# Kernel optimization log

Hardware: AMD Instinct MI355X
Metric: run time of the kernel (lower is better)

The kernel has to match this reference:

```python
import jax, jax.numpy as jnp
import numpy as np

N_EMB = 256
HEAD_SIZE = 256
B, T = 8, 4096

def setup_inputs() -> dict:
    key = jax.random.key(0)
    kx, kk, kq, kv = jax.random.split(key, 4)
    scale = 1.0 / np.sqrt(N_EMB)
    return {
        "x": jax.random.normal(kx, (B, T, N_EMB), dtype=jnp.float32),
        # torch Linear(n_emb, head_size, bias=False): weight [head_size, n_emb], y = x @ W.T
        # store transposed as [n_emb, head_size]
        "Wk": jax.random.normal(kk, (N_EMB, HEAD_SIZE), dtype=jnp.float32) * scale,
        "Wq": jax.random.normal(kq, (N_EMB, HEAD_SIZE), dtype=jnp.float32) * scale,
        "Wv": jax.random.normal(kv, (N_EMB, HEAD_SIZE), dtype=jnp.float32) * scale,
    }

def reference(x, Wk, Wq, Wv):
    # x: [B, T, n_emb]
    k = x @ Wk  # [B, T, H]
    q = x @ Wq
    v = x @ Wv
    T_ = x.shape[1]
    scores = jnp.einsum("bqh,bkh->bqk", q, k) * (N_EMB ** -0.5)  # note: scaled by n_emb, as in source
    causal = jnp.tril(jnp.ones((T_, T_), dtype=bool))
    scores = jnp.where(causal, scores, -jnp.inf)
    attn = jax.nn.softmax(scores, axis=-1)
    return attn @ v  # [B, T, H]
```

## Files before the change

kernel.cpp:

```cpp
#include <hip/hip_runtime.h>

#define Bn 8
#define Tn 4096
#define Dn 256
#define Mn (Bn*Tn)

typedef short bf16x8 __attribute__((ext_vector_type(8)));
typedef float f32x4 __attribute__((ext_vector_type(4)));
typedef float f32x16 __attribute__((ext_vector_type(16)));

#define P_OFF   0ul
#define ML_OFF  41943040ul
#define XB_OFF  0ul
#define WT_OFF  16777216ul
#define QKV_OFF 42598400ul

__device__ __forceinline__ unsigned short f2bf(float f) {
    union { float f; unsigned int u; } v; v.f = f;
    unsigned int r = v.u + 0x7fffu + ((v.u >> 16) & 1u);
    return (unsigned short)(r >> 16);
}
__device__ __forceinline__ float bf2f(unsigned short u) {
    union { unsigned int u; float f; } v; v.u = ((unsigned int)u) << 16;
    return v.f;
}
__device__ __forceinline__ unsigned int pk2(float a, float b) {
    return (unsigned int)f2bf(a) | ((unsigned int)f2bf(b) << 16);
}

typedef __attribute__((address_space(1))) const unsigned int* gas_p;
typedef __attribute__((address_space(3))) unsigned int* las_p;
__device__ __forceinline__ void g2lds16(const void* g, void* l) {
    __builtin_amdgcn_global_load_lds((gas_p)g, (las_p)l, 16, 0, 0);
}

__global__ void __launch_bounds__(256) cast_x_kernel(const float* __restrict__ x,
                                                     unsigned short* __restrict__ xb) {
    size_t i = (size_t)blockIdx.x * 256 + threadIdx.x;
    const float4* p = reinterpret_cast<const float4*>(x) + i * 2;
    float4 a = p[0], b = p[1];
    union { unsigned short u[8]; uint4 v; } o;
    o.u[0]=f2bf(a.x); o.u[1]=f2bf(a.y); o.u[2]=f2bf(a.z); o.u[3]=f2bf(a.w);
    o.u[4]=f2bf(b.x); o.u[5]=f2bf(b.y); o.u[6]=f2bf(b.z); o.u[7]=f2bf(b.w);
    reinterpret_cast<uint4*>(xb)[i] = o.v;
}

__global__ void __launch_bounds__(256) wt_kernel(const float* __restrict__ wq,
                                                 const float* __restrict__ wk,
                                                 const float* __restrict__ wv,
                                                 unsigned short* __restrict__ wt) {
    int idx = blockIdx.x * 256 + threadIdx.x;
    int h = idx >> 16; int r = idx & 65535;
    int k = r >> 8, n = r & 255;
    const float* src = (h == 0) ? wq : (h == 1) ? wk : wv;
    wt[h * 65536 + n * 256 + k] = f2bf(src[k * 256 + n]);
}

__global__ void __launch_bounds__(256, 2) proj_kernel(const unsigned short* __restrict__ xb,
                                                      const unsigned short* __restrict__ wt,
                                                      unsigned short* __restrict__ qkv) {
    __shared__ unsigned short wlds[256 * 40];
    int h = blockIdx.y;
    const unsigned short* wth = wt + h * 65536;
    int m0 = blockIdx.x * 64;
    int tid = threadIdx.x;
    int w = tid >> 6, lane = tid & 63;
    int c = lane & 15, g = lane >> 4;
    size_t arow = (size_t)(m0 + w * 16 + c);

    const f32x4 fz = {0.f, 0.f, 0.f, 0.f};
    f32x4 acc[16];
#pragma unroll
    for (int n = 0; n < 16; n++) acc[n] = fz;

    for (int kk = 0; kk < 8; kk++) {
        __syncthreads();
#pragma unroll
        for (int p = 0; p < 4; p++) {
            int idx = p * 256 + tid;
            int r = idx >> 2, ch = idx & 3;
            bf16x8 v = *(const bf16x8*)(wth + r * 256 + kk * 32 + ch * 8);
            *(bf16x8*)(&wlds[r * 40 + ch * 8]) = v;
        }
        __syncthreads();
        bf16x8 af = *(const bf16x8*)(xb + arow * Dn + kk * 32 + g * 8);
#pragma unroll
        for (int n = 0; n < 16; n++) {
            bf16x8 bfv = *(const bf16x8*)(&wlds[(n * 16 + c) * 40 + g * 8]);
            acc[n] = __builtin_amdgcn_mfma_f32_16x16x32_bf16(af, bfv, acc[n], 0, 0, 0);
        }
    }
    int orow0 = m0 + w * 16 + g * 4;
    if (h < 2) {
        unsigned short* out = qkv + (size_t)h * Mn * Dn;
#pragma unroll
        for (int n = 0; n < 16; n++)
#pragma unroll
            for (int r = 0; r < 4; r++)
                out[(size_t)(orow0 + r) * Dn + n * 16 + c] = f2bf(acc[n][r]);
    } else {
        unsigned short* vt = qkv + (size_t)2 * Mn * Dn;
#pragma unroll
        for (int n = 0; n < 16; n++) {
            union { unsigned short u[4]; ushort4 v4; } pk;
#pragma unroll
            for (int r = 0; r < 4; r++) pk.u[r] = f2bf(acc[n][r]);
            *(ushort4*)(vt + (size_t)(n * 16 + c) * Mn + orow0) = pk.v4;
        }
    }
}

__global__ void __launch_bounds__(256, 2) attn_kernel(const unsigned short* __restrict__ qkv,
                                                      unsigned short* __restrict__ part,
                                                      float2* __restrict__ ml) {
    __shared__ char smem[65536];

    int bid = blockIdx.x;
    int b = bid & 7;
    int r = bid >> 3;
    int qtp, cc;
    if (r < 24)      { qtp = 24 + (r & 7); cc = r >> 3; }
    else if (r < 40) { int rp = r - 24; qtp = 16 + (rp & 7); cc = rp >> 3; }
    else if (r < 48) { qtp = 8 + (r - 40); cc = 0; }
    else             { int k = r - 48; int u = k >> 2, v = k & 3; qtp = 8 * v + 7 - u; cc = v; }
    int slot = b * 80 + r;

    int tid = threadIdx.x, w = tid >> 6, lane = tid & 63;
    int lq = lane & 31, hh = lane >> 5;

    const unsigned short* Qg = qkv;
    const unsigned short* Kg = qkv + (size_t)Mn * Dn;
    const unsigned short* Vt = qkv + (size_t)2 * Mn * Dn;

    int qrow = qtp * 128 + w * 32 + lq;

    bf16x8 qf[16];
#pragma unroll
    for (int s = 0; s < 16; s++)
        qf[s] = *(const bf16x8*)(Qg + ((size_t)b * Tn + qrow) * Dn + s * 16 + hh * 8);

    f32x16 o[8];
#pragma unroll
    for (int dg = 0; dg < 8; dg++)
#pragma unroll
        for (int e = 0; e < 16; e++) o[dg][e] = 0.f;
    float m2 = -INFINITY, lsum = 0.f;

    const float C1 = 0.09016844005555897f;

    auto STAGE = [&](int bufsel, int t) {
        const unsigned short* kgb = Kg + ((size_t)b * Tn + t * 32) * Dn;
        char* kb = smem + bufsel * 32768 + w * 4096;
#pragma unroll
        for (int i = 0; i < 4; i++) {
            int row = w * 8 + i * 2 + hh;
            int chunk = lq ^ row;
            g2lds16(kgb + row * 256 + chunk * 8, kb + i * 1024);
        }
        const unsigned short* vgb = Vt + (size_t)b * Tn + t * 32;
        char* vb = smem + bufsel * 32768 + 16384 + w * 4096;
#pragma unroll
        for (int i = 0; i < 4; i++) {
            int d = w * 64 + i * 16 + (lane >> 2);
            int kvc = (lane & 3) ^ ((d >> 3) & 3);
            g2lds16(vgb + (size_t)d * Mn + kvc * 8, vb + i * 1024);
        }
    };

    auto COMPUTE = [&](int bufsel, int t) {
        int kv0 = t * 32;
        const char* klds = smem + bufsel * 32768;
        const char* vlds = klds + 16384;
        f32x16 sv;
#pragma unroll
        for (int e = 0; e < 16; e++) sv[e] = 0.f;
        __builtin_amdgcn_s_setprio(1);
#pragma unroll
        for (int s = 0; s < 16; s++) {
            bf16x8 kf = *(const bf16x8*)(klds + lq * 512 + ((2 * s + hh) ^ lq) * 16);
            sv = __builtin_amdgcn_mfma_f32_32x32x16_bf16(kf, qf[s], sv, 0, 0, 0);
        }
        __builtin_amdgcn_s_setprio(0);
        float pv[16];
        float tmax = -INFINITY;
#pragma unroll
        for (int rr = 0; rr < 16; rr++) {
            int kvl = kv0 + (rr & 3) + 8 * (rr >> 2) + 4 * hh;
            float v = sv[rr] * C1;
            v = (kvl <= qrow) ? v : -INFINITY;
            pv[rr] = v;
            tmax = fmaxf(tmax, v);
        }
        tmax = fmaxf(tmax, __shfl_xor(tmax, 32));
        float mn = m2;
        if (!__all(tmax - m2 <= 8.0f)) {
            mn = fmaxf(m2, tmax);
            float alpha = exp2f(m2 - mn);
            lsum *= alpha;
            m2 = mn;
#pragma unroll
            for (int dg = 0; dg < 8; dg++) o[dg] = o[dg] * alpha;
        }
        float ps = 0.f;
#pragma unroll
        for (int rr = 0; rr < 16; rr++) {
            pv[rr] = exp2f(pv[rr] - mn);
            ps += pv[rr];
        }
        ps += __shfl_xor(ps, 32);
        lsum += ps;
        union U4 { unsigned int u[4]; bf16x8 v; };
        U4 fr[2];
#pragma unroll
        for (int s2 = 0; s2 < 2; s2++) {
            int bidx = 8 * s2;
            unsigned int w0 = pk2(pv[bidx + 0], pv[bidx + 1]);
            unsigned int w1 = pk2(pv[bidx + 2], pv[bidx + 3]);
            unsigned int y0 = pk2(pv[bidx + 4], pv[bidx + 5]);
            unsigned int y1 = pk2(pv[bidx + 6], pv[bidx + 7]);
            unsigned int e0 = hh ? w0 : y0;
            unsigned int e1 = hh ? w1 : y1;
            unsigned int x0 = (unsigned int)__shfl_xor((int)e0, 32);
            unsigned int x1 = (unsigned int)__shfl_xor((int)e1, 32);
            fr[s2].u[0] = hh ? x0 : w0;
            fr[s2].u[1] = hh ? x1 : w1;
            fr[s2].u[2] = hh ? y0 : x0;
            fr[s2].u[3] = hh ? y1 : x1;
        }
        __builtin_amdgcn_s_setprio(1);
#pragma unroll
        for (int dg = 0; dg < 8; dg++) {
            int d = 32 * dg + lq;
            int swz = (d >> 3) & 3;
#pragma unroll
            for (int s2 = 0; s2 < 2; s2++) {
                bf16x8 vf = *(const bf16x8*)(vlds + d * 64 + ((2 * s2 + hh) ^ swz) * 16);
                o[dg] = __builtin_amdgcn_mfma_f32_32x32x16_bf16(vf, fr[s2].v, o[dg], 0, 0, 0);
            }
        }
        __builtin_amdgcn_s_setprio(0);
    };

    int t0 = cc * 32;
    int tend = min(t0 + 32, 4 * (qtp + 1));
    int cur = 0;
    STAGE(0, t0);
    __syncthreads();
    for (int t = t0; t < tend; t++) {
        if (t + 1 < tend) STAGE(cur ^ 1, t + 1);
        COMPUTE(cur, t);
        __syncthreads();
        cur ^= 1;
    }

    if (hh == 0)
        ml[(size_t)slot * 128 + w * 32 + lq] = make_float2(m2, lsum);

    uint4* pb = (uint4*)part;
#pragma unroll
    for (int dg = 0; dg < 8; dg++) {
        uint4 lo, hi2;
        lo.x = pk2(o[dg][0], o[dg][1]);  lo.y = pk2(o[dg][2], o[dg][3]);
        lo.z = pk2(o[dg][4], o[dg][5]);  lo.w = pk2(o[dg][6], o[dg][7]);
        hi2.x = pk2(o[dg][8], o[dg][9]);  hi2.y = pk2(o[dg][10], o[dg][11]);
        hi2.z = pk2(o[dg][12], o[dg][13]); hi2.w = pk2(o[dg][14], o[dg][15]);
        size_t base = (size_t)slot * 4096 + w * 1024 + dg * 128 + lane;
        pb[base] = lo;
        pb[base + 64] = hi2;
    }
}

__global__ void __launch_bounds__(256) combine_kernel(const unsigned short* __restrict__ part,
                                                      const float2* __restrict__ ml,
                                                      float* __restrict__ out) {
    __shared__ float2 mls[4][32];
    int bid = blockIdx.x;
    int b = bid & 7;
    int rest = bid >> 3;
    int qtp = rest >> 2, w = rest & 3;
    int nch = (qtp >> 3) + 1;
    int tid = threadIdx.x;

    int slots[4];
#pragma unroll
    for (int ci = 0; ci < 4; ci++) {
        int rr;
        if (ci == nch - 1)       rr = 48 + 4 * (7 - (qtp & 7)) + (qtp >> 3);
        else if (qtp >= 24)      rr = 8 * ci + (qtp - 24);
        else if (qtp >= 16)      rr = 24 + 8 * ci + (qtp - 16);
        else                     rr = 40 + (qtp - 8);
        slots[ci] = b * 80 + rr;
    }
    if (tid < nch * 32) {
        int ci = tid >> 5, qq = tid & 31;
        mls[ci][qq] = ml[(size_t)slots[ci] * 128 + w * 32 + qq];
    }
    __syncthreads();

    int dg = tid >> 5, h2 = (tid >> 4) & 1, ls = tid & 15;
    const uint4* pb = (const uint4*)part;

    for (int rd = 0; rd < 4; rd++) {
        int lane_idx = ls + 16 * rd;
        int q = lane_idx & 31, hh = lane_idx >> 5;
        float M = -INFINITY;
#pragma unroll
        for (int ci = 0; ci < 4; ci++)
            if (ci < nch) M = fmaxf(M, mls[ci][q].x);
        float L = 0.f, wgt[4];
#pragma unroll
        for (int ci = 0; ci < 4; ci++) {
            if (ci < nch) { wgt[ci] = exp2f(mls[ci][q].x - M); L += wgt[ci] * mls[ci][q].y; }
            else wgt[ci] = 0.f;
        }
        float inv = 1.f / L;
        float a[8];
#pragma unroll
        for (int e = 0; e < 8; e++) a[e] = 0.f;
#pragma unroll
        for (int ci = 0; ci < 4; ci++) {
            if (ci >= nch) break;
            uint4 u = pb[(size_t)slots[ci] * 4096 + w * 1024 + dg * 128 + h2 * 64 + lane_idx];
            float wg = wgt[ci];
            a[0] += wg * bf2f((unsigned short)(u.x & 0xffff));
            a[1] += wg * bf2f((unsigned short)(u.x >> 16));
            a[2] += wg * bf2f((unsigned short)(u.y & 0xffff));
            a[3] += wg * bf2f((unsigned short)(u.y >> 16));
            a[4] += wg * bf2f((unsigned short)(u.z & 0xffff));
            a[5] += wg * bf2f((unsigned short)(u.z >> 16));
            a[6] += wg * bf2f((unsigned short)(u.w & 0xffff));
            a[7] += wg * bf2f((unsigned short)(u.w >> 16));
        }
        size_t row = (size_t)b * Tn + qtp * 128 + w * 32 + q;
        int dbase = 32 * dg + 16 * h2 + 4 * hh;
        float4 A = {a[0] * inv, a[1] * inv, a[2] * inv, a[3] * inv};
        float4 Bv = {a[4] * inv, a[5] * inv, a[6] * inv, a[7] * inv};
        *(float4*)(out + row * 256 + dbase) = A;
        *(float4*)(out + row * 256 + dbase + 8) = Bv;
    }
}

extern "C" void kernel_launch(void* const* d_in, const int* in_sizes, int n_in,
                              void* d_out, int out_size, void* d_ws, size_t ws_size,
                              hipStream_t stream) {
    (void)in_sizes; (void)n_in; (void)out_size; (void)ws_size;
    const float* x  = (const float*)d_in[0];
    const float* wk = (const float*)d_in[1];
    const float* wq = (const float*)d_in[2];
    const float* wv = (const float*)d_in[3];
    float* outp = (float*)d_out;

    char* ws = (char*)d_ws;
    unsigned short* xb   = (unsigned short*)(ws + XB_OFF);
    unsigned short* wt   = (unsigned short*)(ws + WT_OFF);
    unsigned short* qkv  = (unsigned short*)(ws + QKV_OFF);
    unsigned short* part = (unsigned short*)(ws + P_OFF);
    float2*         mlp  = (float2*)(ws + ML_OFF);

    cast_x_kernel<<<Mn * Dn / 8 / 256, 256, 0, stream>>>(x, xb);
    wt_kernel<<<3 * 65536 / 256, 256, 0, stream>>>(wq, wk, wv, wt);
    proj_kernel<<<dim3(Mn / 64, 3), 256, 0, stream>>>(xb, wt, qkv);
    attn_kernel<<<640, 256, 0, stream>>>(qkv, part, mlp);
    combine_kernel<<<1024, 256, 0, stream>>>(part, mlp, outp);
}
```

Baseline: 201.1 us.

## Fuse x cast into projection and single-buffer V to raise attention occupancy

Removes the separate fp32-to-bf16 cast kernel for x and converts x on the fly inside the projection kernel, dropping one launch and a round trip through memory. The attention kernel keeps double-buffered K but single-buffers V, cutting shared memory from 64KB to 48KB so launch bounds allow three blocks per CU. V staging is now serialized behind the PV step with an extra barrier. The QK dot product is split into two independent accumulator chains for more MFMA overlap. The gain from extra occupancy may be offset by lost V prefetch overlap, the added sync, and register pressure at three blocks per CU.

```diff
diff --git a/kernel.cpp b/kernel.cpp
--- a/kernel.cpp
+++ b/kernel.cpp
@@ -11,7 +11,6 @@
 
 #define P_OFF   0ul
 #define ML_OFF  41943040ul
-#define XB_OFF  0ul
 #define WT_OFF  16777216ul
 #define QKV_OFF 42598400ul
 
@@ -32,17 +31,6 @@
 typedef __attribute__((address_space(3))) unsigned int* las_p;
 __device__ __forceinline__ void g2lds16(const void* g, void* l) {
     __builtin_amdgcn_global_load_lds((gas_p)g, (las_p)l, 16, 0, 0);
-}
-
-__global__ void __launch_bounds__(256) cast_x_kernel(const float* __restrict__ x,
-                                                     unsigned short* __restrict__ xb) {
-    size_t i = (size_t)blockIdx.x * 256 + threadIdx.x;
-    const float4* p = reinterpret_cast<const float4*>(x) + i * 2;
-    float4 a = p[0], b = p[1];
-    union { unsigned short u[8]; uint4 v; } o;
-    o.u[0]=f2bf(a.x); o.u[1]=f2bf(a.y); o.u[2]=f2bf(a.z); o.u[3]=f2bf(a.w);
-    o.u[4]=f2bf(b.x); o.u[5]=f2bf(b.y); o.u[6]=f2bf(b.z); o.u[7]=f2bf(b.w);
-    reinterpret_cast<uint4*>(xb)[i] = o.v;
 }
 
 __global__ void __launch_bounds__(256) wt_kernel(const float* __restrict__ wq,
@@ -56,7 +44,7 @@
     wt[h * 65536 + n * 256 + k] = f2bf(src[k * 256 + n]);
 }
 
-__global__ void __launch_bounds__(256, 2) proj_kernel(const unsigned short* __restrict__ xb,
+__global__ void __launch_bounds__(256, 2) proj_kernel(const float* __restrict__ x,
                                                       const unsigned short* __restrict__ wt,
                                                       unsigned short* __restrict__ qkv) {
     __shared__ unsigned short wlds[256 * 40];
@@ -83,11 +71,15 @@
             *(bf16x8*)(&wlds[r * 40 + ch * 8]) = v;
         }
         __syncthreads();
-        bf16x8 af = *(const bf16x8*)(xb + arow * Dn + kk * 32 + g * 8);
+        const float4* xa = (const float4*)(x + arow * Dn + kk * 32 + g * 8);
+        float4 a0 = xa[0], a1 = xa[1];
+        union { unsigned short u[8]; bf16x8 v; } af;
+        af.u[0]=f2bf(a0.x); af.u[1]=f2bf(a0.y); af.u[2]=f2bf(a0.z); af.u[3]=f2bf(a0.w);
+        af.u[4]=f2bf(a1.x); af.u[5]=f2bf(a1.y); af.u[6]=f2bf(a1.z); af.u[7]=f2bf(a1.w);
 #pragma unroll
         for (int n = 0; n < 16; n++) {
             bf16x8 bfv = *(const bf16x8*)(&wlds[(n * 16 + c) * 40 + g * 8]);
-            acc[n] = __builtin_amdgcn_mfma_f32_16x16x32_bf16(af, bfv, acc[n], 0, 0, 0);
+            acc[n] = __builtin_amdgcn_mfma_f32_16x16x32_bf16(af.v, bfv, acc[n], 0, 0, 0);
         }
     }
     int orow0 = m0 + w * 16 + g * 4;
@@ -110,10 +102,10 @@
     }
 }
 
-__global__ void __launch_bounds__(256, 2) attn_kernel(const unsigned short* __restrict__ qkv,
+__global__ void __launch_bounds__(256, 3) attn_kernel(const unsigned short* __restrict__ qkv,
                                                       unsigned short* __restrict__ part,
                                                       float2* __restrict__ ml) {
-    __shared__ char smem[65536];
+    __shared__ char smem[49152];
 
     int bid = blockIdx.x;
     int b = bid & 7;
@@ -148,17 +140,19 @@
 
     const float C1 = 0.09016844005555897f;
 
-    auto STAGE = [&](int bufsel, int t) {
+    auto STAGE_K = [&](int cb, int t) {
         const unsigned short* kgb = Kg + ((size_t)b * Tn + t * 32) * Dn;
-        char* kb = smem + bufsel * 32768 + w * 4096;
+        char* kb = smem + cb * 16384 + w * 4096;
 #pragma unroll
         for (int i = 0; i < 4; i++) {
             int row = w * 8 + i * 2 + hh;
             int chunk = lq ^ row;
             g2lds16(kgb + row * 256 + chunk * 8, kb + i * 1024);
         }
+    };
+    auto STAGE_V = [&](int t) {
         const unsigned short* vgb = Vt + (size_t)b * Tn + t * 32;
-        char* vb = smem + bufsel * 32768 + 16384 + w * 4096;
+        char* vb = smem + 32768 + w * 4096;
 #pragma unroll
         for (int i = 0; i < 4; i++) {
             int d = w * 64 + i * 16 + (lane >> 2);
@@ -167,20 +161,25 @@
         }
     };
 
-    auto COMPUTE = [&](int bufsel, int t) {
+    union U4 { unsigned int u[4]; bf16x8 v; };
+    U4 fr[2];
+
+    auto QKSM = [&](int cb, int t) {
         int kv0 = t * 32;
-        const char* klds = smem + bufsel * 32768;
-        const char* vlds = klds + 16384;
-        f32x16 sv;
-#pragma unroll
-        for (int e = 0; e < 16; e++) sv[e] = 0.f;
+        const char* klds = smem + cb * 16384;
+        f32x16 sva, svb;
+#pragma unroll
+        for (int e = 0; e < 16; e++) { sva[e] = 0.f; svb[e] = 0.f; }
         __builtin_amdgcn_s_setprio(1);
 #pragma unroll
-        for (int s = 0; s < 16; s++) {
-            bf16x8 kf = *(const bf16x8*)(klds + lq * 512 + ((2 * s + hh) ^ lq) * 16);
-            sv = __builtin_amdgcn_mfma_f32_32x32x16_bf16(kf, qf[s], sv, 0, 0, 0);
+        for (int s = 0; s < 8; s++) {
+            bf16x8 kfa = *(const bf16x8*)(klds + lq * 512 + ((2 * s + hh) ^ lq) * 16);
+            sva = __builtin_amdgcn_mfma_f32_32x32x16_bf16(kfa, qf[s], sva, 0, 0, 0);
+            bf16x8 kfb = *(const bf16x8*)(klds + lq * 512 + ((2 * (s + 8) + hh) ^ lq) * 16);
+            svb = __builtin_amdgcn_mfma_f32_32x32x16_bf16(kfb, qf[s + 8], svb, 0, 0, 0);
         }
         __builtin_amdgcn_s_setprio(0);
+        f32x16 sv = sva + svb;
         float pv[16];
         float tmax = -INFINITY;
 #pragma unroll
@@ -209,8 +208,6 @@
         }
         ps += __shfl_xor(ps, 32);
         lsum += ps;
-        union U4 { unsigned int u[4]; bf16x8 v; };
-        U4 fr[2];
 #pragma unroll
         for (int s2 = 0; s2 < 2; s2++) {
             int bidx = 8 * s2;
@@ -227,6 +224,10 @@
             fr[s2].u[2] = hh ? y0 : x0;
             fr[s2].u[3] = hh ? y1 : x1;
         }
+    };
+
+    auto PV = [&]() {
+        const char* vlds = smem + 32768;
         __builtin_amdgcn_s_setprio(1);
 #pragma unroll
         for (int dg = 0; dg < 8; dg++) {
@@ -243,14 +244,20 @@
 
     int t0 = cc * 32;
     int tend = min(t0 + 32, 4 * (qtp + 1));
-    int cur = 0;
-    STAGE(0, t0);
+    int cb = 0;
+    STAGE_K(0, t0);
+    STAGE_V(t0);
     __syncthreads();
     for (int t = t0; t < tend; t++) {
-        if (t + 1 < tend) STAGE(cur ^ 1, t + 1);
-        COMPUTE(cur, t);
+        if (t + 1 < tend) STAGE_K(cb ^ 1, t + 1);
+        QKSM(cb, t);
         __syncthreads();
-        cur ^= 1;
+        PV();
+        if (t + 1 < tend) {
+            __syncthreads();
+            STAGE_V(t + 1);
+        }
+        cb ^= 1;
     }
 
     if (hh == 0)
@@ -351,15 +358,13 @@
     float* outp = (float*)d_out;
 
     char* ws = (char*)d_ws;
-    unsigned short* xb   = (unsigned short*)(ws + XB_OFF);
     unsigned short* wt   = (unsigned short*)(ws + WT_OFF);
     unsigned short* qkv  = (unsigned short*)(ws + QKV_OFF);
     unsigned short* part = (unsigned short*)(ws + P_OFF);
     float2*         mlp  = (float2*)(ws + ML_OFF);
 
-    cast_x_kernel<<<Mn * Dn / 8 / 256, 256, 0, stream>>>(x, xb);
     wt_kernel<<<3 * 65536 / 256, 256, 0, stream>>>(wq, wk, wv, wt);
-    proj_kernel<<<dim3(Mn / 64, 3), 256, 0, stream>>>(xb, wt, qkv);
+    proj_kernel<<<dim3(Mn / 64, 3), 256, 0, stream>>>(x, wt, qkv);
     attn_kernel<<<640, 256, 0, stream>>>(qkv, part, mlp);
     combine_kernel<<<1024, 256, 0, stream>>>(part, mlp, outp);
 }
```

Result: slower. 575.9 us (+186.4%).

## Fuse x bf16 cast into projection kernel and compute Q/K/V per block

Applied to the files above, without the earlier changes.

Removes the separate cast_x kernel. Each projection block now loads its 64 fp32 rows of x, converts them to bf16 into padded LDS once, and loops over all three weight matrices instead of using a grid y-dimension of 3. This removes one launch and the bf16 round trip of x through global memory, and stops x being reread once per head. The cost is about 33KB of LDS per block for the x tile, which may limit occupancy, and one third as many blocks each doing three times the work.

```diff
diff --git a/kernel.cpp b/kernel.cpp
--- a/kernel.cpp
+++ b/kernel.cpp
@@ -11,7 +11,6 @@
 
 #define P_OFF   0ul
 #define ML_OFF  41943040ul
-#define XB_OFF  0ul
 #define WT_OFF  16777216ul
 #define QKV_OFF 42598400ul
 
@@ -32,17 +31,6 @@
 typedef __attribute__((address_space(3))) unsigned int* las_p;
 __device__ __forceinline__ void g2lds16(const void* g, void* l) {
     __builtin_amdgcn_global_load_lds((gas_p)g, (las_p)l, 16, 0, 0);
-}
-
-__global__ void __launch_bounds__(256) cast_x_kernel(const float* __restrict__ x,
-                                                     unsigned short* __restrict__ xb) {
-    size_t i = (size_t)blockIdx.x * 256 + threadIdx.x;
-    const float4* p = reinterpret_cast<const float4*>(x) + i * 2;
-    float4 a = p[0], b = p[1];
-    union { unsigned short u[8]; uint4 v; } o;
-    o.u[0]=f2bf(a.x); o.u[1]=f2bf(a.y); o.u[2]=f2bf(a.z); o.u[3]=f2bf(a.w);
-    o.u[4]=f2bf(b.x); o.u[5]=f2bf(b.y); o.u[6]=f2bf(b.z); o.u[7]=f2bf(b.w);
-    reinterpret_cast<uint4*>(xb)[i] = o.v;
 }
 
 __global__ void __launch_bounds__(256) wt_kernel(const float* __restrict__ wq,
@@ -56,56 +44,68 @@
     wt[h * 65536 + n * 256 + k] = f2bf(src[k * 256 + n]);
 }
 
-__global__ void __launch_bounds__(256, 2) proj_kernel(const unsigned short* __restrict__ xb,
+__global__ void __launch_bounds__(256, 2) proj_kernel(const float* __restrict__ x,
                                                       const unsigned short* __restrict__ wt,
                                                       unsigned short* __restrict__ qkv) {
+    __shared__ unsigned short xlds[64 * 258];
     __shared__ unsigned short wlds[256 * 40];
-    int h = blockIdx.y;
-    const unsigned short* wth = wt + h * 65536;
     int m0 = blockIdx.x * 64;
     int tid = threadIdx.x;
     int w = tid >> 6, lane = tid & 63;
     int c = lane & 15, g = lane >> 4;
-    size_t arow = (size_t)(m0 + w * 16 + c);
+
+#pragma unroll
+    for (int it = 0; it < 16; it++) {
+        int idx = it * 256 + tid;
+        int row = idx >> 6, col4 = (idx & 63) * 4;
+        float4 a = *(const float4*)(x + (size_t)(m0 + row) * Dn + col4);
+        union { unsigned short u[4]; ushort4 v4; } o4;
+        o4.u[0] = f2bf(a.x); o4.u[1] = f2bf(a.y); o4.u[2] = f2bf(a.z); o4.u[3] = f2bf(a.w);
+        *(ushort4*)(&xlds[row * 258 + col4]) = o4.v4;
+    }
+    __syncthreads();
 
     const f32x4 fz = {0.f, 0.f, 0.f, 0.f};
-    f32x4 acc[16];
-#pragma unroll
-    for (int n = 0; n < 16; n++) acc[n] = fz;
-
-    for (int kk = 0; kk < 8; kk++) {
-        __syncthreads();
-#pragma unroll
-        for (int p = 0; p < 4; p++) {
-            int idx = p * 256 + tid;
-            int r = idx >> 2, ch = idx & 3;
-            bf16x8 v = *(const bf16x8*)(wth + r * 256 + kk * 32 + ch * 8);
-            *(bf16x8*)(&wlds[r * 40 + ch * 8]) = v;
-        }
-        __syncthreads();
-        bf16x8 af = *(const bf16x8*)(xb + arow * Dn + kk * 32 + g * 8);
-#pragma unroll
-        for (int n = 0; n < 16; n++) {
-            bf16x8 bfv = *(const bf16x8*)(&wlds[(n * 16 + c) * 40 + g * 8]);
-            acc[n] = __builtin_amdgcn_mfma_f32_16x16x32_bf16(af, bfv, acc[n], 0, 0, 0);
-        }
-    }
-    int orow0 = m0 + w * 16 + g * 4;
-    if (h < 2) {
-        unsigned short* out = qkv + (size_t)h * Mn * Dn;
-#pragma unroll
-        for (int n = 0; n < 16; n++)
-#pragma unroll
-            for (int r = 0; r < 4; r++)
-                out[(size_t)(orow0 + r) * Dn + n * 16 + c] = f2bf(acc[n][r]);
-    } else {
-        unsigned short* vt = qkv + (size_t)2 * Mn * Dn;
-#pragma unroll
-        for (int n = 0; n < 16; n++) {
-            union { unsigned short u[4]; ushort4 v4; } pk;
-#pragma unroll
-            for (int r = 0; r < 4; r++) pk.u[r] = f2bf(acc[n][r]);
-            *(ushort4*)(vt + (size_t)(n * 16 + c) * Mn + orow0) = pk.v4;
+    for (int h = 0; h < 3; h++) {
+        const unsigned short* wth = wt + h * 65536;
+        f32x4 acc[16];
+#pragma unroll
+        for (int n = 0; n < 16; n++) acc[n] = fz;
+
+        for (int kk = 0; kk < 8; kk++) {
+            __syncthreads();
+#pragma unroll
+            for (int p = 0; p < 4; p++) {
+                int idx = p * 256 + tid;
+                int r = idx >> 2, ch = idx & 3;
+                bf16x8 v = *(const bf16x8*)(wth + r * 256 + kk * 32 + ch * 8);
+                *(bf16x8*)(&wlds[r * 40 + ch * 8]) = v;
+            }
+            __syncthreads();
+            bf16x8 af = *(const bf16x8*)(&xlds[(w * 16 + c) * 258 + kk * 32 + g * 8]);
+#pragma unroll
+            for (int n = 0; n < 16; n++) {
+                bf16x8 bfv = *(const bf16x8*)(&wlds[(n * 16 + c) * 40 + g * 8]);
+                acc[n] = __builtin_amdgcn_mfma_f32_16x16x32_bf16(af, bfv, acc[n], 0, 0, 0);
+            }
+        }
+        int orow0 = m0 + w * 16 + g * 4;
+        if (h < 2) {
+            unsigned short* out = qkv + (size_t)h * Mn * Dn;
+#pragma unroll
+            for (int n = 0; n < 16; n++)
+#pragma unroll
+                for (int r = 0; r < 4; r++)
+                    out[(size_t)(orow0 + r) * Dn + n * 16 + c] = f2bf(acc[n][r]);
+        } else {
+            unsigned short* vt = qkv + (size_t)2 * Mn * Dn;
+#pragma unroll
+            for (int n = 0; n < 16; n++) {
+                union { unsigned short u[4]; ushort4 v4; } pk;
+#pragma unroll
+                for (int r = 0; r < 4; r++) pk.u[r] = f2bf(acc[n][r]);
+                *(ushort4*)(vt + (size_t)(n * 16 + c) * Mn + orow0) = pk.v4;
+            }
         }
     }
 }
@@ -351,15 +351,13 @@
     float* outp = (float*)d_out;
 
     char* ws = (char*)d_ws;
-    unsigned short* xb   = (unsigned short*)(ws + XB_OFF);
     unsigned short* wt   = (unsigned short*)(ws + WT_OFF);
     unsigned short* qkv  = (unsigned short*)(ws + QKV_OFF);
     unsigned short* part = (unsigned short*)(ws + P_OFF);
     float2*         mlp  = (float2*)(ws + ML_OFF);
 
-    cast_x_kernel<<<Mn * Dn / 8 / 256, 256, 0, stream>>>(x, xb);
     wt_kernel<<<3 * 65536 / 256, 256, 0, stream>>>(wq, wk, wv, wt);
-    proj_kernel<<<dim3(Mn / 64, 3), 256, 0, stream>>>(xb, wt, qkv);
+    proj_kernel<<<Mn / 64, 256, 0, stream>>>(x, wt, qkv);
     attn_kernel<<<640, 256, 0, stream>>>(qkv, part, mlp);
     combine_kernel<<<1024, 256, 0, stream>>>(part, mlp, outp);
 }
```

Result: no change. 198.4 us (-1.3%).
